# Kernel optimization log

Hardware: AMD Instinct MI355X
Metric: run time of the kernel (lower is better)

Reference implementation:

```python
import jax, jax.numpy as jnp
import numpy as np

N_EMBD = 1024
N_HEAD = 16
BASE_SCALE = 0.03125  # config.base_scale
ATTN_ALPHA_INIT = 0.05
MLP_ALPHA_INIT = 0.05
SQK_INIT = 1.0
SUV_INIT = 1.0


def justnorm(x):
    return x / jnp.linalg.norm(x, axis=-1, keepdims=True)


def normalized_linear(x, W):
    # F.normalize(weight, p=2, dim=0): unit-norm columns of W [out, in] across the out dim
    Wn = W / jnp.linalg.norm(W, axis=0, keepdims=True)
    return x @ Wn.T


def setup_inputs() -> dict:
    key = jax.random.key(0)
    ks = jax.random.split(key, 8)
    C = N_EMBD
    s = 1.0 / np.sqrt(C)
    inp = {
        "h": jax.random.normal(ks[0], (8, 1024, C), dtype=jnp.float32),
        "Wq": jax.random.normal(ks[1], (C, C), dtype=jnp.float32) * s,
        "Wk": jax.random.normal(ks[2], (C, C), dtype=jnp.float32) * s,
        "Wv": jax.random.normal(ks[3], (C, C), dtype=jnp.float32) * s,
        "Wo": jax.random.normal(ks[4], (C, C), dtype=jnp.float32) * s,
        "Wfc": jax.random.normal(ks[5], (8 * C, C), dtype=jnp.float32) * s,
        "Wproj": jax.random.normal(ks[6], (C, 4 * C), dtype=jnp.float32) * (1.0 / np.sqrt(4 * C)),
        "sqk": jnp.full((C,), SQK_INIT * BASE_SCALE, dtype=jnp.float32),
        "suv": jnp.full((8 * C,), SUV_INIT * 1.0, dtype=jnp.float32),
        "attn_alpha": jnp.full((C,), BASE_SCALE, dtype=jnp.float32),
        "mlp_alpha": jnp.full((C,), BASE_SCALE, dtype=jnp.float32),
    }
    return inp


def reference(h, Wq, Wk, Wv, Wo, Wfc, Wproj, sqk, suv, attn_alpha, mlp_alpha):
    B, T, C = h.shape
    H, D = N_HEAD, C // N_HEAD

    # ---- attention ----
    q = normalized_linear(h, Wq).reshape(B, T, H, D).transpose(0, 2, 1, 3)  # bhtd
    k = normalized_linear(h, Wk).reshape(B, T, H, D).transpose(0, 2, 1, 3)
    v = normalized_linear(h, Wv).reshape(B, T, H, D).transpose(0, 2, 1, 3)

    sqk_s = (sqk * (SQK_INIT / BASE_SCALE)).reshape(1, H, 1, D)  # per-(head, head_dim) scale
    q = sqk_s * justnorm(q)
    k = sqk_s * justnorm(k)

    softmax_scale = float(D) ** 0.5  # nGPT uses sqrt(head_dim)
    att = jax.nn.softmax(jnp.einsum("bhqd,bhkd->bhqk", q, k) * softmax_scale, axis=-1)
    y = jnp.einsum("bhqk,bhkd->bhqd", att, v)
    y = y.transpose(0, 2, 1, 3).reshape(B, T, C)
    h_att = normalized_linear(y, Wo)

    lr = jnp.abs(attn_alpha * (ATTN_ALPHA_INIT / BASE_SCALE))
    A = justnorm(h)
    Bn = justnorm(h_att)
    h = justnorm(A + lr * (Bn - A))

    # ---- SwiGLU MLP ----
    uv = h @ Wfc.T  # [B,T,8C]
    suv_s = suv * (SUV_INIT / 1.0 * (C ** 0.5))
    uv = suv_s * uv
    u, vg = jnp.split(uv, 2, axis=-1)
    x_mlp = u * jax.nn.silu(vg)
    h_mlp = x_mlp @ Wproj.T

    lr = jnp.abs(mlp_alpha * (MLP_ALPHA_INIT / BASE_SCALE))
    A = justnorm(h)
    Bn = justnorm(h_mlp)
    h = justnorm(A + lr * (Bn - A))
    return h
```

## Files before the change

kernel.cpp:

```cpp
#include <hip/hip_runtime.h>

typedef __attribute__((ext_vector_type(8))) short s8v;
typedef __attribute__((ext_vector_type(4))) short s4v;
typedef __attribute__((ext_vector_type(4))) float f4v;

#define MFMA __builtin_amdgcn_mfma_f32_16x16x32_bf16

__device__ __forceinline__ float b2f(unsigned short b) {
  union { unsigned u; float f; } x; x.u = ((unsigned)b) << 16; return x.f;
}
__device__ __forceinline__ unsigned short f2b(float f) {
  union { float f; unsigned u; } x; x.f = f;
  unsigned r = x.u + 0x7fffu + ((x.u >> 16) & 1u);
  return (unsigned short)(r >> 16);
}
__device__ __forceinline__ void gl_lds16(const void* g, void* l) {
  __builtin_amdgcn_global_load_lds(
      (const __attribute__((address_space(1))) unsigned int*)g,
      (__attribute__((address_space(3))) unsigned int*)l, 16, 0, 0);
}

__global__ void colsq(const float* __restrict__ W, float* __restrict__ out, int K) {
  int j = blockIdx.x * 256 + threadIdx.x;
  const float* p = W + (long)(blockIdx.y * 64) * K + j;
  float s = 0.f;
#pragma unroll 4
  for (int n = 0; n < 64; ++n) { float v = p[(long)n * K]; s += v * v; }
  atomicAdd(&out[j], s);
}

__global__ void convw(const float* __restrict__ src, const float* __restrict__ cs,
                      unsigned short* __restrict__ dst, int Kmask) {
  long idx = ((long)blockIdx.x * 256 + threadIdx.x) << 2;
  float4 v = *(const float4*)(src + idx);
  int j = (int)(idx & (long)Kmask);
  s4v o;
  o[0] = (short)f2b(v.x * rsqrtf(cs[j]));
  o[1] = (short)f2b(v.y * rsqrtf(cs[j + 1]));
  o[2] = (short)f2b(v.z * rsqrtf(cs[j + 2]));
  o[3] = (short)f2b(v.w * rsqrtf(cs[j + 3]));
  *(s4v*)(dst + idx) = o;
}

__global__ void castf2b(const float* __restrict__ src, unsigned short* __restrict__ dst) {
  long idx = ((long)blockIdx.x * 256 + threadIdx.x) << 2;
  float4 v = *(const float4*)(src + idx);
  s4v o;
  o[0] = (short)f2b(v.x); o[1] = (short)f2b(v.y);
  o[2] = (short)f2b(v.z); o[3] = (short)f2b(v.w);
  *(s4v*)(dst + idx) = o;
}

__global__ __launch_bounds__(256) void gemm_bt(
    const unsigned short* __restrict__ A, const unsigned short* __restrict__ B,
    unsigned short* __restrict__ Cout, int K, int ldc) {
  __shared__ unsigned short smem[32768];
  const int tid = threadIdx.x, lane = tid & 63, w = tid >> 6;
  const int quad = lane >> 4, lq = lane & 15;
  const int wy = w >> 1, wx = w & 1;
  const int m0 = blockIdx.y << 7, n0 = blockIdx.x << 7;

  const int trow = tid >> 2;
  const int cb = ((tid & 3) ^ ((tid >> 3) & 3)) << 3;
  const unsigned short* Ag0 = A + (long)(m0 + trow) * K + cb;
  const unsigned short* Ag1 = A + (long)(m0 + 64 + trow) * K + cb;
  const unsigned short* Bg0 = B + (long)(n0 + trow) * K + cb;
  const unsigned short* Bg1 = B + (long)(n0 + 64 + trow) * K + cb;
  unsigned short* l0 = smem + (tid << 3);

  const int swz = ((lq >> 1) & 3) << 4;
  const int aoff = (wy * 64 + lq) * 64 + ((quad << 4) ^ swz);
  const int boff = 8192 + (wx * 64 + lq) * 64 + ((quad << 4) ^ swz);

  f4v acc[4][4];
  f4v zero = {0.f, 0.f, 0.f, 0.f};
#pragma unroll
  for (int i = 0; i < 4; ++i)
#pragma unroll
    for (int j = 0; j < 4; ++j) acc[i][j] = zero;

  auto stage = [&](int T) {
    const int bo = (T & 3) << 13;
    const int col = T << 5;
    gl_lds16(Ag0 + col, l0 + bo);
    gl_lds16(Ag1 + col, l0 + bo + 2048);
    gl_lds16(Bg0 + col, l0 + bo + 4096);
    gl_lds16(Bg1 + col, l0 + bo + 6144);
  };
  const char* sb = (const char*)smem;
  auto compute = [&](int kt) {
    const int bo = (kt & 3) << 14;
    s8v a[4], b[4];
#pragma unroll
    for (int i = 0; i < 4; ++i) a[i] = *(const s8v*)(sb + bo + aoff + i * 1024);
#pragma unroll
    for (int j = 0; j < 4; ++j) b[j] = *(const s8v*)(sb + bo + boff + j * 1024);
    __builtin_amdgcn_s_setprio(1);
#pragma unroll
    for (int i = 0; i < 4; ++i)
#pragma unroll
      for (int j = 0; j < 4; ++j)
        acc[i][j] = MFMA(a[i], b[j], acc[i][j], 0, 0, 0);
    __builtin_amdgcn_s_setprio(0);
  };

  const int nt = K >> 5;
  stage(0); stage(1); stage(2);
  for (int kt = 0; kt < nt - 2; ++kt) {
    asm volatile("s_waitcnt vmcnt(8)" ::: "memory");
    __builtin_amdgcn_s_barrier();
    asm volatile("" ::: "memory");
    if (kt < nt - 3) stage(kt + 3);
    compute(kt);
  }
  asm volatile("s_waitcnt vmcnt(4)" ::: "memory");
  __builtin_amdgcn_s_barrier();
  asm volatile("" ::: "memory");
  compute(nt - 2);
  asm volatile("s_waitcnt vmcnt(0)" ::: "memory");
  __builtin_amdgcn_s_barrier();
  asm volatile("" ::: "memory");
  compute(nt - 1);

  __syncthreads();
#pragma unroll
  for (int i = 0; i < 4; ++i)
#pragma unroll
    for (int j = 0; j < 4; ++j)
#pragma unroll
      for (int r = 0; r < 4; ++r) {
        int row = wy * 64 + i * 16 + quad * 4 + r;
        int col = wx * 64 + j * 16 + lq;
        smem[row * 136 + col] = f2b(acc[i][j][r]);
      }
  __syncthreads();
#pragma unroll
  for (int it = 0; it < 8; ++it) {
    int row = it * 16 + (tid >> 4);
    int col = (tid & 15) << 3;
    s8v v = *(const s8v*)(smem + row * 136 + col);
    *(s8v*)(Cout + (long)(m0 + row) * ldc + n0 + col) = v;
  }
}

__global__ __launch_bounds__(512, 2) void gemm_fc(
    const unsigned short* __restrict__ A, const unsigned short* __restrict__ B,
    unsigned short* __restrict__ X, const float* __restrict__ suv) {
  __shared__ unsigned short smem[65536];
  const int tid = threadIdx.x, lane = tid & 63, w = tid >> 6;
  const int quad = lane >> 4, lq = lane & 15;
  const int wy = w >> 2, wx = w & 3;
  const int bid = blockIdx.x;
  const int xr = bid & 7, xq = bid >> 3;
  const int m0 = ((xr << 2) | (xq & 3)) << 8;
  const int n0 = (xq >> 2) << 7;

  const int trow = tid >> 3;
  const int scol = ((tid & 7) ^ (trow & 7)) << 3;
  const unsigned short* pA = A + (long)(m0 + trow) * 1024 + scol;
  const unsigned short* pB = B + (long)(n0 + trow) * 1024 + scol;
  unsigned short* ldst = smem + tid * 8;

  auto stA = [&](int tile, int half) {
    const int base = (tile & 1) * 32768 + half * 8192;
    const unsigned short* src = pA + (long)half * 131072 + (tile << 6);
    gl_lds16(src, ldst + base);
    gl_lds16(src + 65536, ldst + base + 4096);
  };
  auto stB = [&](int tile, int vh) {
    const int base = (tile & 1) * 32768 + 16384 + vh * 8192;
    const unsigned short* src = pB + (long)vh * 4194304 + (tile << 6);
    gl_lds16(src, ldst + base);
    gl_lds16(src + 65536, ldst + base + 4096);
  };

  const int rsw = (lq & 7) << 4;
  const int c0 = (quad * 16) ^ rsw;
  const int c1 = (64 + quad * 16) ^ rsw;
  const int aro = wy * 16384 + lq * 128;
  const int uro = 32768 + (wx * 32 + lq) * 128;
  const int vro = 49152 + (wx * 32 + lq) * 128;
  const char* sb = (const char*)smem;

  f4v aU[8][2], aV[8][2];
  f4v zero = {0.f, 0.f, 0.f, 0.f};
#pragma unroll
  for (int m = 0; m < 8; ++m)
#pragma unroll
    for (int j = 0; j < 2; ++j) { aU[m][j] = zero; aV[m][j] = zero; }

  s8v av[4][2], uf[2][2], vg[2][2];

  auto tile_phases = [&](int t, int bufB) {
#pragma unroll
    for (int m = 0; m < 4; ++m) {
      av[m][0] = *(const s8v*)(sb + bufB + aro + m * 2048 + c0);
      av[m][1] = *(const s8v*)(sb + bufB + aro + m * 2048 + c1);
    }
#pragma unroll
    for (int j = 0; j < 2; ++j) {
      uf[j][0] = *(const s8v*)(sb + bufB + uro + j * 2048 + c0);
      uf[j][1] = *(const s8v*)(sb + bufB + uro + j * 2048 + c1);
    }
    if (t < 15) stA(t + 1, 1);
    __builtin_amdgcn_s_barrier();
    asm volatile("" ::: "memory");
    __builtin_amdgcn_s_setprio(1);
#pragma unroll
    for (int m = 0; m < 4; ++m)
#pragma unroll
      for (int j = 0; j < 2; ++j) {
        aU[m][j] = MFMA(av[m][0], uf[j][0], aU[m][j], 0, 0, 0);
        aU[m][j] = MFMA(av[m][1], uf[j][1], aU[m][j], 0, 0, 0);
      }
    __builtin_amdgcn_s_setprio(0);
    asm volatile("" ::: "memory");
    __builtin_amdgcn_s_barrier();
    asm volatile("" ::: "memory");
#pragma unroll
    for (int j = 0; j < 2; ++j) {
      vg[j][0] = *(const s8v*)(sb + bufB + vro + j * 2048 + c0);
      vg[j][1] = *(const s8v*)(sb + bufB + vro + j * 2048 + c1);
    }
    if (t < 14) stB(t + 2, 0);
    __builtin_amdgcn_s_barrier();
    asm volatile("" ::: "memory");
    __builtin_amdgcn_s_setprio(1);
#pragma unroll
    for (int m = 0; m < 4; ++m)
#pragma unroll
      for (int j = 0; j < 2; ++j) {
        aV[m][j] = MFMA(av[m][0], vg[j][0], aV[m][j], 0, 0, 0);
        aV[m][j] = MFMA(av[m][1], vg[j][1], aV[m][j], 0, 0, 0);
      }
    __builtin_amdgcn_s_setprio(0);
    asm volatile("" ::: "memory");
    __builtin_amdgcn_s_barrier();
    asm volatile("" ::: "memory");
#pragma unroll
    for (int m = 0; m < 4; ++m) {
      av[m][0] = *(const s8v*)(sb + bufB + aro + (m + 4) * 2048 + c0);
      av[m][1] = *(const s8v*)(sb + bufB + aro + (m + 4) * 2048 + c1);
    }
    if (t < 14) stB(t + 2, 1);
    __builtin_amdgcn_s_barrier();
    asm volatile("" ::: "memory");
    __builtin_amdgcn_s_setprio(1);
#pragma unroll
    for (int m = 0; m < 4; ++m)
#pragma unroll
      for (int j = 0; j < 2; ++j) {
        aU[m + 4][j] = MFMA(av[m][0], uf[j][0], aU[m + 4][j], 0, 0, 0);
        aU[m + 4][j] = MFMA(av[m][1], uf[j][1], aU[m + 4][j], 0, 0, 0);
      }
    __builtin_amdgcn_s_setprio(0);
    asm volatile("" ::: "memory");
    __builtin_amdgcn_s_barrier();
    asm volatile("" ::: "memory");
    if (t < 14) stA(t + 2, 0);
    __builtin_amdgcn_s_barrier();
    asm volatile("" ::: "memory");
    __builtin_amdgcn_s_setprio(1);
#pragma unroll
    for (int m = 0; m < 4; ++m)
#pragma unroll
      for (int j = 0; j < 2; ++j) {
        aV[m + 4][j] = MFMA(av[m][0], vg[j][0], aV[m + 4][j], 0, 0, 0);
        aV[m + 4][j] = MFMA(av[m][1], vg[j][1], aV[m + 4][j], 0, 0, 0);
      }
    __builtin_amdgcn_s_setprio(0);
    if (t < 14) { asm volatile("s_waitcnt vmcnt(6)" ::: "memory"); }
    else if (t == 14) { asm volatile("s_waitcnt vmcnt(0)" ::: "memory"); }
    asm volatile("" ::: "memory");
    __builtin_amdgcn_s_barrier();
    asm volatile("" ::: "memory");
  };

  stB(0, 0); stB(0, 1); stA(0, 0); stA(0, 1);
  stB(1, 0); stB(1, 1); stA(1, 0);
  asm volatile("s_waitcnt vmcnt(6)" ::: "memory");
  __builtin_amdgcn_s_barrier();
  asm volatile("" ::: "memory");

  for (int tt = 0; tt < 8; ++tt) {
    tile_phases(tt * 2, 0);
    tile_phases(tt * 2 + 1, 65536);
  }

  float su[2], sv[2];
#pragma unroll
  for (int j = 0; j < 2; ++j) {
    su[j] = suv[n0 + wx * 32 + j * 16 + lq] * 32.f;
    sv[j] = suv[4096 + n0 + wx * 32 + j * 16 + lq] * 32.f;
  }
  __syncthreads();
#pragma unroll
  for (int m = 0; m < 8; ++m)
#pragma unroll
    for (int j = 0; j < 2; ++j)
#pragma unroll
      for (int r = 0; r < 4; ++r) {
        int row = wy * 128 + m * 16 + quad * 4 + r;
        int col = wx * 32 + j * 16 + lq;
        float uu = aU[m][j][r] * su[j];
        float vv = aV[m][j][r] * sv[j];
        float sig = 1.f / (1.f + __builtin_amdgcn_exp2f(vv * -1.44269504f));
        smem[row * 132 + col] = f2b(uu * vv * sig);
      }
  __syncthreads();
  {
    const int row = tid >> 1, half = tid & 1;
    unsigned short* dst = X + (long)(m0 + row) * 4096 + n0 + half * 64;
    const unsigned short* srcr = smem + row * 132 + half * 64;
#pragma unroll
    for (int s = 0; s < 8; ++s)
      *(s8v*)(dst + s * 8) = *(const s8v*)(srcr + s * 8);
  }
}

__global__ __launch_bounds__(256) void qkv_norm(unsigned short* __restrict__ qkv,
                                                unsigned short* __restrict__ Vt,
                                                const float* __restrict__ sqk) {
  __shared__ unsigned short tl[64][72];
  const int tid = threadIdx.x;
  const int blk = blockIdx.x;
  const int tt = blk & 15, bh = blk >> 4, b = bh >> 4, h = bh & 15;
  const int t0 = tt << 6;
  const int r = tid >> 2, seg = tid & 3;
  float sc[16];
#pragma unroll
  for (int c = 0; c < 16; ++c) sc[c] = sqk[h * 64 + seg * 16 + c] * 32.f;
  for (int which = 0; which < 2; ++which) {
    unsigned short* p = qkv + (long)(b * 1024 + t0 + r) * 3072 + which * 1024 + h * 64 + seg * 16;
    s8v x0 = *(const s8v*)p, x1 = *(const s8v*)(p + 8);
    float ss = 0.f;
#pragma unroll
    for (int c = 0; c < 8; ++c) {
      float a = b2f((unsigned short)x0[c]), bb = b2f((unsigned short)x1[c]);
      ss += a * a + bb * bb;
    }
    ss += __shfl_xor(ss, 1, 64);
    ss += __shfl_xor(ss, 2, 64);
    float rn = rsqrtf(ss);
#pragma unroll
    for (int c = 0; c < 8; ++c) {
      x0[c] = (short)f2b(b2f((unsigned short)x0[c]) * rn * sc[c]);
      x1[c] = (short)f2b(b2f((unsigned short)x1[c]) * rn * sc[c + 8]);
    }
    *(s8v*)p = x0; *(s8v*)(p + 8) = x1;
  }
  {
    const unsigned short* p = qkv + (long)(b * 1024 + t0 + r) * 3072 + 2048 + h * 64 + seg * 16;
    s8v v0 = *(const s8v*)p, v1 = *(const s8v*)(p + 8);
#pragma unroll
    for (int c = 0; c < 8; ++c) {
      tl[seg * 16 + c][r] = (unsigned short)v0[c];
      tl[seg * 16 + 8 + c][r] = (unsigned short)v1[c];
    }
  }
  __syncthreads();
  {
    const int d = tid >> 2, part = tid & 3;
    s8v o0 = *(const s8v*)(&tl[d][part * 16]);
    s8v o1 = *(const s8v*)(&tl[d][part * 16 + 8]);
    unsigned short* q = Vt + (long)(bh * 64 + d) * 1024 + t0 + part * 16;
    *(s8v*)q = o0; *(s8v*)(q + 8) = o1;
  }
}

__global__ __launch_bounds__(256) void attn(const unsigned short* __restrict__ qkv,
                                            const unsigned short* __restrict__ Vt,
                                            unsigned short* __restrict__ Y) {
  __shared__ unsigned short smem[33792];
  unsigned short* Klds = smem;
  unsigned short* Vlds = smem + 8192;
  unsigned short* Plds = smem + 16384;
  const int tid = threadIdx.x, lane = tid & 63, w = tid >> 6;
  const int quad = lane >> 4, lq = lane & 15;
  const int bh = blockIdx.x, b = bh >> 4, h = bh & 15;
  const int qt = blockIdx.y;
  const int e0 = tid << 3;
  const int c_lo = e0 >> 10, row_s = (e0 & 1023) >> 3;
  const int vc_lo = e0 >> 9, vd = (e0 & 511) >> 3;

  s8v qf[2][2];
#pragma unroll
  for (int i = 0; i < 2; ++i)
#pragma unroll
    for (int ks = 0; ks < 2; ++ks) {
      int row = qt * 128 + w * 32 + i * 16 + lq;
      qf[i][ks] = *(const s8v*)(qkv + (long)(b * 1024 + row) * 3072 + h * 64 + ks * 32 + quad * 8);
    }

  f4v o[2][4];
  float lp[2][4];
  f4v zero = {0.f, 0.f, 0.f, 0.f};
#pragma unroll
  for (int i = 0; i < 2; ++i) {
#pragma unroll
    for (int nf = 0; nf < 4; ++nf) o[i][nf] = zero;
#pragma unroll
    for (int r = 0; r < 4; ++r) lp[i][r] = 0.f;
  }

  const unsigned short* Kg = qkv + (long)(b * 1024 + row_s) * 3072 + 1024 + h * 64 + (c_lo << 3);
  const unsigned short* Vg = Vt + (long)(bh * 64 + vd) * 1024 + (vc_lo << 3);
  unsigned short* Pw = Plds + w * 4352;

  for (int kt0 = 0; kt0 < 1024; kt0 += 128) {
    __syncthreads();
#pragma unroll
    for (int it = 0; it < 4; ++it) {
      gl_lds16(Kg + (long)kt0 * 3072 + it * 16, Klds + it * 2048 + e0);
      gl_lds16(Vg + kt0 + it * 32, Vlds + it * 2048 + e0);
    }
    __syncthreads();
    f4v s[2][8];
#pragma unroll
    for (int i = 0; i < 2; ++i)
#pragma unroll
      for (int j = 0; j < 8; ++j) s[i][j] = zero;
#pragma unroll
    for (int ks = 0; ks < 2; ++ks)
#pragma unroll
      for (int j = 0; j < 8; ++j) {
        s8v kf = *(const s8v*)(Klds + (ks * 4 + quad) * 1024 + (j * 16 + lq) * 8);
        s[0][j] = MFMA(qf[0][ks], kf, s[0][j], 0, 0, 0);
        s[1][j] = MFMA(qf[1][ks], kf, s[1][j], 0, 0, 0);
      }
#pragma unroll
    for (int i = 0; i < 2; ++i)
#pragma unroll
      for (int j = 0; j < 8; ++j)
#pragma unroll
        for (int r = 0; r < 4; ++r) {
          float p = __builtin_amdgcn_exp2f(s[i][j][r] * 11.5415603f - 11.5415603f);
          lp[i][r] += p;
          Pw[(i * 16 + quad * 4 + r) * 136 + j * 16 + lq] = f2b(p);
        }
    s8v pf[2][4];
#pragma unroll
    for (int i = 0; i < 2; ++i)
#pragma unroll
      for (int ks = 0; ks < 4; ++ks)
        pf[i][ks] = *(const s8v*)(Pw + (i * 16 + lq) * 136 + ks * 32 + quad * 8);
#pragma unroll
    for (int nf = 0; nf < 4; ++nf)
#pragma unroll
      for (int ks = 0; ks < 4; ++ks) {
        s8v vf = *(const s8v*)(Vlds + (ks * 4 + quad) * 512 + (nf * 16 + lq) * 8);
        o[0][nf] = MFMA(pf[0][ks], vf, o[0][nf], 0, 0, 0);
        o[1][nf] = MFMA(pf[1][ks], vf, o[1][nf], 0, 0, 0);
      }
  }
#pragma unroll
  for (int i = 0; i < 2; ++i)
#pragma unroll
    for (int r = 0; r < 4; ++r) {
      float v = lp[i][r];
      v += __shfl_xor(v, 1, 64); v += __shfl_xor(v, 2, 64);
      v += __shfl_xor(v, 4, 64); v += __shfl_xor(v, 8, 64);
      lp[i][r] = 1.f / v;
    }
#pragma unroll
  for (int i = 0; i < 2; ++i)
#pragma unroll
    for (int nf = 0; nf < 4; ++nf)
#pragma unroll
      for (int r = 0; r < 4; ++r) {
        int row = qt * 128 + w * 32 + i * 16 + quad * 4 + r;
        Y[(long)(b * 1024 + row) * 1024 + h * 64 + nf * 16 + lq] = f2b(o[i][nf][r] * lp[i][r]);
      }
}

__global__ __launch_bounds__(256) void residual(
    const float* __restrict__ hin, const unsigned short* __restrict__ hbr,
    const float* __restrict__ alpha, float* __restrict__ outf,
    unsigned short* __restrict__ outb) {
  __shared__ float red[8];
  const int tid = threadIdx.x, lane = tid & 63, w = tid >> 6;
  const long base = (long)blockIdx.x * 1024;
  float hv[4], bvv[4];
  float s1 = 0.f, s2 = 0.f;
#pragma unroll
  for (int k = 0; k < 4; ++k) {
    int c = k * 256 + tid;
    hv[k] = hin[base + c];
    bvv[k] = b2f(hbr[base + c]);
    s1 += hv[k] * hv[k]; s2 += bvv[k] * bvv[k];
  }
#pragma unroll
  for (int m = 1; m < 64; m <<= 1) { s1 += __shfl_xor(s1, m, 64); s2 += __shfl_xor(s2, m, 64); }
  if (lane == 0) { red[w] = s1; red[4 + w] = s2; }
  __syncthreads();
  s1 = red[0] + red[1] + red[2] + red[3];
  s2 = red[4] + red[5] + red[6] + red[7];
  float rn1 = rsqrtf(s1), rn2 = rsqrtf(s2);
  float z[4], s3 = 0.f;
#pragma unroll
  for (int k = 0; k < 4; ++k) {
    int c = k * 256 + tid;
    float a = hv[k] * rn1;
    float lr = fabsf(alpha[c]) * 1.6f;
    float zz = a + lr * (bvv[k] * rn2 - a);
    z[k] = zz; s3 += zz * zz;
  }
#pragma unroll
  for (int m = 1; m < 64; m <<= 1) s3 += __shfl_xor(s3, m, 64);
  __syncthreads();
  if (lane == 0) red[w] = s3;
  __syncthreads();
  s3 = red[0] + red[1] + red[2] + red[3];
  float rn3 = rsqrtf(s3);
#pragma unroll
  for (int k = 0; k < 4; ++k) {
    int c = k * 256 + tid;
    float ov = z[k] * rn3;
    if (outf) outf[base + c] = ov;
    if (outb) outb[base + c] = f2b(ov);
  }
}

extern "C" void kernel_launch(void* const* d_in, const int* in_sizes, int n_in,
                              void* d_out, int out_size, void* d_ws, size_t ws_size,
                              hipStream_t stream) {
  const float* h   = (const float*)d_in[0];
  const float* Wq  = (const float*)d_in[1];
  const float* Wk  = (const float*)d_in[2];
  const float* Wv  = (const float*)d_in[3];
  const float* Wo  = (const float*)d_in[4];
  const float* Wfc = (const float*)d_in[5];
  const float* Wpj = (const float*)d_in[6];
  const float* sqk = (const float*)d_in[7];
  const float* suv = (const float*)d_in[8];
  const float* aat = (const float*)d_in[9];
  const float* aml = (const float*)d_in[10];
  float* out = (float*)d_out;

  char* ws = (char*)d_ws;
  size_t off = 0;
  auto alloc = [&](size_t n) { char* p = ws + off; off += (n + 255) & ~(size_t)255; return p; };
  float* cs_q  = (float*)alloc(4096);
  float* cs_k  = (float*)alloc(4096);
  float* cs_v  = (float*)alloc(4096);
  float* cs_o  = (float*)alloc(4096);
  unsigned short* Wqkv_b = (unsigned short*)alloc(3ull * 1024 * 1024 * 2);
  unsigned short* Wo_b   = (unsigned short*)alloc(1024ull * 1024 * 2);
  unsigned short* Wfc_b  = (unsigned short*)alloc(8192ull * 1024 * 2);
  unsigned short* Wpj_b  = (unsigned short*)alloc(1024ull * 4096 * 2);
  unsigned short* slotC  = (unsigned short*)alloc(8192ull * 1024 * 2);
  unsigned short* slotD  = (unsigned short*)alloc(8192ull * 4096 * 2);
  unsigned short* slotE  = (unsigned short*)alloc(8192ull * 1024 * 2);
  unsigned short* y_b    = (unsigned short*)alloc(8192ull * 1024 * 2);
  float*          h2_f   = (float*)alloc(8192ull * 1024 * 4);

  unsigned short* h_b    = slotC;
  unsigned short* hmlp_b = slotC;
  unsigned short* qkv_r  = slotD;
  unsigned short* xmlp   = slotD;
  unsigned short* hatt_b = slotD + 25165824;
  unsigned short* Vt     = slotE;
  unsigned short* h2_b   = slotE;

  hipMemsetAsync(ws, 0, 16384, stream);
  colsq<<<dim3(4, 16), 256, 0, stream>>>(Wq, cs_q, 1024);
  colsq<<<dim3(4, 16), 256, 0, stream>>>(Wk, cs_k, 1024);
  colsq<<<dim3(4, 16), 256, 0, stream>>>(Wv, cs_v, 1024);
  colsq<<<dim3(4, 16), 256, 0, stream>>>(Wo, cs_o, 1024);
  convw<<<1024, 256, 0, stream>>>(Wq, cs_q, Wqkv_b, 1023);
  convw<<<1024, 256, 0, stream>>>(Wk, cs_k, Wqkv_b + 1048576, 1023);
  convw<<<1024, 256, 0, stream>>>(Wv, cs_v, Wqkv_b + 2097152, 1023);
  convw<<<1024, 256, 0, stream>>>(Wo, cs_o, Wo_b, 1023);
  castf2b<<<8192, 256, 0, stream>>>(Wfc, Wfc_b);
  castf2b<<<4096, 256, 0, stream>>>(Wpj, Wpj_b);
  castf2b<<<8192, 256, 0, stream>>>(h, h_b);
  gemm_bt<<<dim3(24, 64), 256, 0, stream>>>(h_b, Wqkv_b, qkv_r, 1024, 3072);
  qkv_norm<<<2048, 256, 0, stream>>>(qkv_r, Vt, sqk);
  attn<<<dim3(128, 8), 256, 0, stream>>>(qkv_r, Vt, y_b);
  gemm_bt<<<dim3(8, 64), 256, 0, stream>>>(y_b, Wo_b, hatt_b, 1024, 1024);
  residual<<<8192, 256, 0, stream>>>(h, hatt_b, aat, h2_f, h2_b);
  gemm_fc<<<1024, 512, 0, stream>>>(h2_b, Wfc_b, xmlp, suv);
  gemm_bt<<<dim3(8, 64), 256, 0, stream>>>(xmlp, Wpj_b, hmlp_b, 4096, 1024);
  residual<<<8192, 256, 0, stream>>>(h2_f, hmlp_b, aml, out, nullptr);
}
```

Before: 642.1 us.

## Double-buffer K tiles in LDS and load V fragments directly to registers

The attention loop now double-buffers K tiles in LDS and prefetches the next K tile while the current one is computed, which removes one of the two barriers per iteration. V fragments are read straight from global memory into registers in MFMA operand layout instead of being staged through LDS. The aim is to hide global load latency behind compute and cut LDS traffic. In exchange it uses more registers for the V fragments, and the vmcnt(0) wait also stalls on the V register loads, which could limit how much overlap is achieved.

```diff
diff --git a/kernel.cpp b/kernel.cpp
--- a/kernel.cpp
+++ b/kernel.cpp
@@ -372,8 +372,6 @@
                                             const unsigned short* __restrict__ Vt,
                                             unsigned short* __restrict__ Y) {
   __shared__ unsigned short smem[33792];
-  unsigned short* Klds = smem;
-  unsigned short* Vlds = smem + 8192;
   unsigned short* Plds = smem + 16384;
   const int tid = threadIdx.x, lane = tid & 63, w = tid >> 6;
   const int quad = lane >> 4, lq = lane & 15;
@@ -381,7 +379,6 @@
   const int qt = blockIdx.y;
   const int e0 = tid << 3;
   const int c_lo = e0 >> 10, row_s = (e0 & 1023) >> 3;
-  const int vc_lo = e0 >> 9, vd = (e0 & 511) >> 3;
 
   s8v qf[2][2];
 #pragma unroll
@@ -404,17 +401,32 @@
   }
 
   const unsigned short* Kg = qkv + (long)(b * 1024 + row_s) * 3072 + 1024 + h * 64 + (c_lo << 3);
-  const unsigned short* Vg = Vt + (long)(bh * 64 + vd) * 1024 + (vc_lo << 3);
+  const unsigned short* Vrow = Vt + ((long)(bh * 64 + lq) * 1024) + quad * 8;
   unsigned short* Pw = Plds + w * 4352;
 
-  for (int kt0 = 0; kt0 < 1024; kt0 += 128) {
-    __syncthreads();
-#pragma unroll
-    for (int it = 0; it < 4; ++it) {
-      gl_lds16(Kg + (long)kt0 * 3072 + it * 16, Klds + it * 2048 + e0);
-      gl_lds16(Vg + kt0 + it * 32, Vlds + it * 2048 + e0);
-    }
-    __syncthreads();
+  auto stageK = [&](int t) {
+    unsigned short* dst = smem + (t & 1) * 8192 + e0;
+    const unsigned short* src = Kg + (long)t * 393216;
+#pragma unroll
+    for (int it = 0; it < 4; ++it)
+      gl_lds16(src + it * 16, dst + it * 2048);
+  };
+
+  stageK(0);
+
+  for (int t = 0; t < 8; ++t) {
+    asm volatile("s_waitcnt vmcnt(0)" ::: "memory");
+    __builtin_amdgcn_s_barrier();
+    asm volatile("" ::: "memory");
+    s8v vf[4][4];
+#pragma unroll
+    for (int nf = 0; nf < 4; ++nf)
+#pragma unroll
+      for (int ks = 0; ks < 4; ++ks)
+        vf[nf][ks] = *(const s8v*)(Vrow + (long)nf * 16384 + t * 128 + ks * 32);
+    if (t < 7) stageK(t + 1);
+
+    const unsigned short* Kl = smem + (t & 1) * 8192;
     f4v s[2][8];
 #pragma unroll
     for (int i = 0; i < 2; ++i)
@@ -424,7 +436,7 @@
     for (int ks = 0; ks < 2; ++ks)
 #pragma unroll
       for (int j = 0; j < 8; ++j) {
-        s8v kf = *(const s8v*)(Klds + (ks * 4 + quad) * 1024 + (j * 16 + lq) * 8);
+        s8v kf = *(const s8v*)(Kl + (ks * 4 + quad) * 1024 + (j * 16 + lq) * 8);
         s[0][j] = MFMA(qf[0][ks], kf, s[0][j], 0, 0, 0);
         s[1][j] = MFMA(qf[1][ks], kf, s[1][j], 0, 0, 0);
       }
@@ -448,9 +460,8 @@
     for (int nf = 0; nf < 4; ++nf)
 #pragma unroll
       for (int ks = 0; ks < 4; ++ks) {
-        s8v vf = *(const s8v*)(Vlds + (ks * 4 + quad) * 512 + (nf * 16 + lq) * 8);
-        o[0][nf] = MFMA(pf[0][ks], vf, o[0][nf], 0, 0, 0);
-        o[1][nf] = MFMA(pf[1][ks], vf, o[1][nf], 0, 0, 0);
+        o[0][nf] = MFMA(pf[0][ks], vf[nf][ks], o[0][nf], 0, 0, 0);
+        o[1][nf] = MFMA(pf[1][ks], vf[nf][ks], o[1][nf], 0, 0, 0);
       }
   }
 #pragma unroll
```

After: 649.7 us. No clear change (+1.2%).

## Fuse q/k head normalization and V transpose into QKV GEMM epilogue; batch prep kernels

Applied to the files above, without the earlier changes.

A specialized QKV GEMM now applies the per-head L2 normalization and sqk scaling to q/k tiles in registers, and writes V tiles transposed directly into the Vt layout. This removes the separate qkv_norm kernel and its extra read and write of the qkv buffer. The separate column-norm, weight-convert and cast launches are also merged into three multi-tensor kernels to cut launch count. The QKV GEMM epilogue normalizes q/k from fp32 accumulators instead of rounded bf16 values, which changes numerics slightly.

```diff
diff --git a/kernel.cpp b/kernel.cpp
--- a/kernel.cpp
+++ b/kernel.cpp
@@ -20,30 +20,44 @@
       (__attribute__((address_space(3))) unsigned int*)l, 16, 0, 0);
 }
 
-__global__ void colsq(const float* __restrict__ W, float* __restrict__ out, int K) {
+__global__ void colsq4(const float* __restrict__ Wq, const float* __restrict__ Wk,
+                       const float* __restrict__ Wv, const float* __restrict__ Wo,
+                       float* __restrict__ cs) {
+  const int z = blockIdx.z;
+  const float* W = (z == 0) ? Wq : (z == 1) ? Wk : (z == 2) ? Wv : Wo;
   int j = blockIdx.x * 256 + threadIdx.x;
-  const float* p = W + (long)(blockIdx.y * 64) * K + j;
+  const float* p = W + (long)(blockIdx.y * 64) * 1024 + j;
   float s = 0.f;
 #pragma unroll 4
-  for (int n = 0; n < 64; ++n) { float v = p[(long)n * K]; s += v * v; }
-  atomicAdd(&out[j], s);
-}
-
-__global__ void convw(const float* __restrict__ src, const float* __restrict__ cs,
-                      unsigned short* __restrict__ dst, int Kmask) {
+  for (int n = 0; n < 64; ++n) { float v = p[(long)n * 1024]; s += v * v; }
+  atomicAdd(&cs[z * 1024 + j], s);
+}
+
+__global__ void convw4(const float* __restrict__ Wq, const float* __restrict__ Wk,
+                       const float* __restrict__ Wv, const float* __restrict__ Wo,
+                       const float* __restrict__ cs, unsigned short* __restrict__ dst) {
+  const int y = blockIdx.y;
+  const float* src = (y == 0) ? Wq : (y == 1) ? Wk : (y == 2) ? Wv : Wo;
   long idx = ((long)blockIdx.x * 256 + threadIdx.x) << 2;
   float4 v = *(const float4*)(src + idx);
-  int j = (int)(idx & (long)Kmask);
+  const float* c = cs + y * 1024 + (int)(idx & 1023);
   s4v o;
-  o[0] = (short)f2b(v.x * rsqrtf(cs[j]));
-  o[1] = (short)f2b(v.y * rsqrtf(cs[j + 1]));
-  o[2] = (short)f2b(v.z * rsqrtf(cs[j + 2]));
-  o[3] = (short)f2b(v.w * rsqrtf(cs[j + 3]));
-  *(s4v*)(dst + idx) = o;
-}
-
-__global__ void castf2b(const float* __restrict__ src, unsigned short* __restrict__ dst) {
-  long idx = ((long)blockIdx.x * 256 + threadIdx.x) << 2;
+  o[0] = (short)f2b(v.x * rsqrtf(c[0]));
+  o[1] = (short)f2b(v.y * rsqrtf(c[1]));
+  o[2] = (short)f2b(v.z * rsqrtf(c[2]));
+  o[3] = (short)f2b(v.w * rsqrtf(c[3]));
+  *(s4v*)(dst + (long)y * 1048576 + idx) = o;
+}
+
+__global__ void cast3(const float* __restrict__ Wfc, const float* __restrict__ Wpj,
+                      const float* __restrict__ h, unsigned short* __restrict__ Wfc_b,
+                      unsigned short* __restrict__ Wpj_b, unsigned short* __restrict__ h_b) {
+  int bid = blockIdx.x;
+  const float* src; unsigned short* dst;
+  if (bid < 8192) { src = Wfc; dst = Wfc_b; }
+  else if (bid < 12288) { src = Wpj; dst = Wpj_b; bid -= 8192; }
+  else { src = h; dst = h_b; bid -= 12288; }
+  long idx = ((long)bid * 256 + threadIdx.x) << 2;
   float4 v = *(const float4*)(src + idx);
   s4v o;
   o[0] = (short)f2b(v.x); o[1] = (short)f2b(v.y);
@@ -143,6 +157,143 @@
   }
 }
 
+__global__ __launch_bounds__(256) void gemm_qkv(
+    const unsigned short* __restrict__ A, const unsigned short* __restrict__ B,
+    unsigned short* __restrict__ Cout, unsigned short* __restrict__ Vt,
+    const float* __restrict__ sqk) {
+  __shared__ unsigned short smem[32768];
+  const int tid = threadIdx.x, lane = tid & 63, w = tid >> 6;
+  const int quad = lane >> 4, lq = lane & 15;
+  const int wy = w >> 1, wx = w & 1;
+  const int m0 = blockIdx.y << 7, n0 = blockIdx.x << 7;
+  const int K = 1024;
+
+  const int trow = tid >> 2;
+  const int cb = ((tid & 3) ^ ((tid >> 3) & 3)) << 3;
+  const unsigned short* Ag0 = A + (long)(m0 + trow) * K + cb;
+  const unsigned short* Ag1 = A + (long)(m0 + 64 + trow) * K + cb;
+  const unsigned short* Bg0 = B + (long)(n0 + trow) * K + cb;
+  const unsigned short* Bg1 = B + (long)(n0 + 64 + trow) * K + cb;
+  unsigned short* l0 = smem + (tid << 3);
+
+  const int swz = ((lq >> 1) & 3) << 4;
+  const int aoff = (wy * 64 + lq) * 64 + ((quad << 4) ^ swz);
+  const int boff = 8192 + (wx * 64 + lq) * 64 + ((quad << 4) ^ swz);
+
+  f4v acc[4][4];
+  f4v zero = {0.f, 0.f, 0.f, 0.f};
+#pragma unroll
+  for (int i = 0; i < 4; ++i)
+#pragma unroll
+    for (int j = 0; j < 4; ++j) acc[i][j] = zero;
+
+  auto stage = [&](int T) {
+    const int bo = (T & 3) << 13;
+    const int col = T << 5;
+    gl_lds16(Ag0 + col, l0 + bo);
+    gl_lds16(Ag1 + col, l0 + bo + 2048);
+    gl_lds16(Bg0 + col, l0 + bo + 4096);
+    gl_lds16(Bg1 + col, l0 + bo + 6144);
+  };
+  const char* sb = (const char*)smem;
+  auto compute = [&](int kt) {
+    const int bo = (kt & 3) << 14;
+    s8v a[4], b[4];
+#pragma unroll
+    for (int i = 0; i < 4; ++i) a[i] = *(const s8v*)(sb + bo + aoff + i * 1024);
+#pragma unroll
+    for (int j = 0; j < 4; ++j) b[j] = *(const s8v*)(sb + bo + boff + j * 1024);
+    __builtin_amdgcn_s_setprio(1);
+#pragma unroll
+    for (int i = 0; i < 4; ++i)
+#pragma unroll
+      for (int j = 0; j < 4; ++j)
+        acc[i][j] = MFMA(a[i], b[j], acc[i][j], 0, 0, 0);
+    __builtin_amdgcn_s_setprio(0);
+  };
+
+  stage(0); stage(1); stage(2);
+  for (int kt = 0; kt < 30; ++kt) {
+    asm volatile("s_waitcnt vmcnt(8)" ::: "memory");
+    __builtin_amdgcn_s_barrier();
+    asm volatile("" ::: "memory");
+    if (kt < 29) stage(kt + 3);
+    compute(kt);
+  }
+  asm volatile("s_waitcnt vmcnt(4)" ::: "memory");
+  __builtin_amdgcn_s_barrier();
+  asm volatile("" ::: "memory");
+  compute(30);
+  asm volatile("s_waitcnt vmcnt(0)" ::: "memory");
+  __builtin_amdgcn_s_barrier();
+  asm volatile("" ::: "memory");
+  compute(31);
+
+  if (n0 < 2048) {
+    float sc[4];
+#pragma unroll
+    for (int j = 0; j < 4; ++j)
+      sc[j] = sqk[(n0 + wx * 64 + j * 16 + lq) & 1023] * 32.f;
+#pragma unroll
+    for (int i = 0; i < 4; ++i)
+#pragma unroll
+      for (int r = 0; r < 4; ++r) {
+        float ss = 0.f;
+#pragma unroll
+        for (int j = 0; j < 4; ++j) ss += acc[i][j][r] * acc[i][j][r];
+        ss += __shfl_xor(ss, 1, 64); ss += __shfl_xor(ss, 2, 64);
+        ss += __shfl_xor(ss, 4, 64); ss += __shfl_xor(ss, 8, 64);
+        float rn = rsqrtf(ss);
+#pragma unroll
+        for (int j = 0; j < 4; ++j) acc[i][j][r] *= rn * sc[j];
+      }
+    __syncthreads();
+#pragma unroll
+    for (int i = 0; i < 4; ++i)
+#pragma unroll
+      for (int j = 0; j < 4; ++j)
+#pragma unroll
+        for (int r = 0; r < 4; ++r) {
+          int row = wy * 64 + i * 16 + quad * 4 + r;
+          int col = wx * 64 + j * 16 + lq;
+          smem[row * 136 + col] = f2b(acc[i][j][r]);
+        }
+    __syncthreads();
+#pragma unroll
+    for (int it = 0; it < 8; ++it) {
+      int row = it * 16 + (tid >> 4);
+      int col = (tid & 15) << 3;
+      s8v v = *(const s8v*)(smem + row * 136 + col);
+      *(s8v*)(Cout + (long)(m0 + row) * 3072 + n0 + col) = v;
+    }
+  } else {
+    __syncthreads();
+#pragma unroll
+    for (int i = 0; i < 4; ++i)
+#pragma unroll
+      for (int j = 0; j < 4; ++j) {
+        int col = wx * 64 + j * 16 + lq;
+        int rowb = wy * 64 + i * 16 + quad * 4;
+        s4v pk;
+#pragma unroll
+        for (int r = 0; r < 4; ++r) pk[r] = (short)f2b(acc[i][j][r]);
+        *(s4v*)(smem + col * 136 + rowb) = pk;
+      }
+    __syncthreads();
+    {
+      const int c = tid >> 1, half = tid & 1;
+      const int f = (n0 - 2048) + c;
+      const int bh = ((m0 >> 10) << 4) + (f >> 6);
+      const int d = f & 63;
+      unsigned short* dst = Vt + (long)(bh * 64 + d) * 1024 + (m0 & 1023) + half * 64;
+      const unsigned short* src = smem + c * 136 + half * 64;
+#pragma unroll
+      for (int s = 0; s < 8; ++s)
+        *(s8v*)(dst + s * 8) = *(const s8v*)(src + s * 8);
+    }
+  }
+}
+
 __global__ __launch_bounds__(512, 2) void gemm_fc(
     const unsigned short* __restrict__ A, const unsigned short* __restrict__ B,
     unsigned short* __restrict__ X, const float* __restrict__ suv) {
@@ -315,56 +466,6 @@
 #pragma unroll
     for (int s = 0; s < 8; ++s)
       *(s8v*)(dst + s * 8) = *(const s8v*)(srcr + s * 8);
-  }
-}
-
-__global__ __launch_bounds__(256) void qkv_norm(unsigned short* __restrict__ qkv,
-                                                unsigned short* __restrict__ Vt,
-                                                const float* __restrict__ sqk) {
-  __shared__ unsigned short tl[64][72];
-  const int tid = threadIdx.x;
-  const int blk = blockIdx.x;
-  const int tt = blk & 15, bh = blk >> 4, b = bh >> 4, h = bh & 15;
-  const int t0 = tt << 6;
-  const int r = tid >> 2, seg = tid & 3;
-  float sc[16];
-#pragma unroll
-  for (int c = 0; c < 16; ++c) sc[c] = sqk[h * 64 + seg * 16 + c] * 32.f;
-  for (int which = 0; which < 2; ++which) {
-    unsigned short* p = qkv + (long)(b * 1024 + t0 + r) * 3072 + which * 1024 + h * 64 + seg * 16;
-    s8v x0 = *(const s8v*)p, x1 = *(const s8v*)(p + 8);
-    float ss = 0.f;
-#pragma unroll
-    for (int c = 0; c < 8; ++c) {
-      float a = b2f((unsigned short)x0[c]), bb = b2f((unsigned short)x1[c]);
-      ss += a * a + bb * bb;
-    }
-    ss += __shfl_xor(ss, 1, 64);
-    ss += __shfl_xor(ss, 2, 64);
-    float rn = rsqrtf(ss);
-#pragma unroll
-    for (int c = 0; c < 8; ++c) {
-      x0[c] = (short)f2b(b2f((unsigned short)x0[c]) * rn * sc[c]);
-      x1[c] = (short)f2b(b2f((unsigned short)x1[c]) * rn * sc[c + 8]);
-    }
-    *(s8v*)p = x0; *(s8v*)(p + 8) = x1;
-  }
-  {
-    const unsigned short* p = qkv + (long)(b * 1024 + t0 + r) * 3072 + 2048 + h * 64 + seg * 16;
-    s8v v0 = *(const s8v*)p, v1 = *(const s8v*)(p + 8);
-#pragma unroll
-    for (int c = 0; c < 8; ++c) {
-      tl[seg * 16 + c][r] = (unsigned short)v0[c];
-      tl[seg * 16 + 8 + c][r] = (unsigned short)v1[c];
-    }
-  }
-  __syncthreads();
-  {
-    const int d = tid >> 2, part = tid & 3;
-    s8v o0 = *(const s8v*)(&tl[d][part * 16]);
-    s8v o1 = *(const s8v*)(&tl[d][part * 16 + 8]);
-    unsigned short* q = Vt + (long)(bh * 64 + d) * 1024 + t0 + part * 16;
-    *(s8v*)q = o0; *(s8v*)(q + 8) = o1;
   }
 }
 
@@ -540,10 +641,7 @@
   char* ws = (char*)d_ws;
   size_t off = 0;
   auto alloc = [&](size_t n) { char* p = ws + off; off += (n + 255) & ~(size_t)255; return p; };
-  float* cs_q  = (float*)alloc(4096);
-  float* cs_k  = (float*)alloc(4096);
-  float* cs_v  = (float*)alloc(4096);
-  float* cs_o  = (float*)alloc(4096);
+  float* cs4   = (float*)alloc(16384);
   unsigned short* Wqkv_b = (unsigned short*)alloc(3ull * 1024 * 1024 * 2);
   unsigned short* Wo_b   = (unsigned short*)alloc(1024ull * 1024 * 2);
   unsigned short* Wfc_b  = (unsigned short*)alloc(8192ull * 1024 * 2);
@@ -563,19 +661,10 @@
   unsigned short* h2_b   = slotE;
 
   hipMemsetAsync(ws, 0, 16384, stream);
-  colsq<<<dim3(4, 16), 256, 0, stream>>>(Wq, cs_q, 1024);
-  colsq<<<dim3(4, 16), 256, 0, stream>>>(Wk, cs_k, 1024);
-  colsq<<<dim3(4, 16), 256, 0, stream>>>(Wv, cs_v, 1024);
-  colsq<<<dim3(4, 16), 256, 0, stream>>>(Wo, cs_o, 1024);
-  convw<<<1024, 256, 0, stream>>>(Wq, cs_q, Wqkv_b, 1023);
-  convw<<<1024, 256, 0, stream>>>(Wk, cs_k, Wqkv_b + 1048576, 1023);
-  convw<<<1024, 256, 0, stream>>>(Wv, cs_v, Wqkv_b + 2097152, 1023);
-  convw<<<1024, 256, 0, stream>>>(Wo, cs_o, Wo_b, 1023);
-  castf2b<<<8192, 256, 0, stream>>>(Wfc, Wfc_b);
-  castf2b<<<4096, 256, 0, stream>>>(Wpj, Wpj_b);
-  castf2b<<<8192, 256, 0, stream>>>(h, h_b);
-  gemm_bt<<<dim3(24, 64), 256, 0, stream>>>(h_b, Wqkv_b, qkv_r, 1024, 3072);
-  qkv_norm<<<2048, 256, 0, stream>>>(qkv_r, Vt, sqk);
+  colsq4<<<dim3(4, 16, 4), 256, 0, stream>>>(Wq, Wk, Wv, Wo, cs4);
+  convw4<<<dim3(1024, 4), 256, 0, stream>>>(Wq, Wk, Wv, Wo, cs4, Wqkv_b);
+  cast3<<<20480, 256, 0, stream>>>(Wfc, Wpj, h, Wfc_b, Wpj_b, h_b);
+  gemm_qkv<<<dim3(24, 64), 256, 0, stream>>>(h_b, Wqkv_b, qkv_r, Vt, sqk);
   attn<<<dim3(128, 8), 256, 0, stream>>>(qkv_r, Vt, y_b);
   gemm_bt<<<dim3(8, 64), 256, 0, stream>>>(y_b, Wo_b, hatt_b, 1024, 1024);
   residual<<<8192, 256, 0, stream>>>(h, hatt_b, aat, h2_f, h2_b);
```

After: 592.2 us. 7.8% less time.
